# Optimization experiments

Hardware: AMD Instinct MI355X
Metric: run time of the kernel (lower is better)

The kernel has to match this reference:

```python
import jax, jax.numpy as jnp
import numpy as np

B, H, S, D = 4, 16, 2048, 128

def setup_inputs() -> dict:
    key = jax.random.key(0)
    kq, kk, kv = jax.random.split(key, 3)
    q = jax.random.normal(kq, (B, H, S, D), dtype=jnp.float32)
    k = jax.random.normal(kk, (B, H, S, D), dtype=jnp.float32)
    v = jax.random.normal(kv, (B, H, S, D), dtype=jnp.float32)
    # causal mask: True = masked (upper triangle above the diagonal)
    mask = jnp.triu(jnp.ones((S, S), dtype=jnp.bool_), k=1)[None, None, :, :]
    return {"q": q, "k": k, "v": v, "mask": mask}

def reference(q, k, v, mask):
    head_dim = q.shape[-1]
    scale = 1.0 / jnp.sqrt(jnp.float32(head_dim))
    # scores: [B, H, Sq, Sk]
    scores = jnp.einsum('bhqd,bhkd->bhqk', q, k) * scale
    scores = jnp.where(mask, -jnp.inf, scores)
    attention_weights = jax.nn.softmax(scores, axis=-1)
    # dropout p=0.0 (eval): identity
    context_vectors = jnp.einsum('bhqk,bhkd->bhqd', attention_weights, v)
    return (context_vectors, attention_weights)
```

## Files before the change

kernel.cpp:

```cpp
#include <hip/hip_runtime.h>
#include <hip/hip_bf16.h>

#define S_LEN 2048
#define D_DIM 128
#define BH_N  64
#define BR    64
#define BC    64
#define NTILE (S_LEN / BC)
#define SCALE 0.08838834764831845f
#define WB    256

typedef __attribute__((ext_vector_type(8)))  short short8;
typedef __attribute__((ext_vector_type(16))) float f32x16;

__device__ __forceinline__ ushort f2bf(float f) {
  union { float f; unsigned u; } x; x.f = f;
  unsigned r = x.u + 0x7FFFu + ((x.u >> 16) & 1u);
  return (ushort)(r >> 16);
}

__device__ __forceinline__ short8 pack8(float4 a, float4 b) {
  short8 p;
  p[0] = (short)f2bf(a.x); p[1] = (short)f2bf(a.y);
  p[2] = (short)f2bf(a.z); p[3] = (short)f2bf(a.w);
  p[4] = (short)f2bf(b.x); p[5] = (short)f2bf(b.y);
  p[6] = (short)f2bf(b.z); p[7] = (short)f2bf(b.w);
  return p;
}

__global__ __launch_bounds__(256, 2) void attn_flash_kernel(
    const float* __restrict__ q, const float* __restrict__ k,
    const float* __restrict__ v, float* __restrict__ ctx,
    float* __restrict__ lsum_out) {
  __shared__ __align__(16) char klds[BC * 256];
  __shared__ __align__(16) char vtlds[D_DIM * 128];
  __shared__ __align__(16) char plds[BR * 128];
  __shared__ float lred[2][BR];

  const int tid  = threadIdx.x;
  const int lane = tid & 63;
  const int w    = tid >> 6;
  const int wq   = w >> 1, wk = w & 1;
  const int l31  = lane & 31, lhi = lane >> 5;

  const int bid = blockIdx.x;
  const int qb  = (NTILE - 1) - (bid >> 6);
  const int bh  = bid & 63;

  const float* qbase = q + (size_t)bh * S_LEN * D_DIM;
  const float* kbase = k + (size_t)bh * S_LEN * D_DIM;
  const float* vbase = v + (size_t)bh * S_LEN * D_DIM;

  short8 qf[8];
  {
    const float* qrow = qbase + (size_t)(qb * BR + wq * 32 + l31) * D_DIM;
    #pragma unroll
    for (int s = 0; s < 8; ++s) {
      int d0 = 16 * s + 8 * lhi;
      float4 a = *(const float4*)(qrow + d0);
      float4 b = *(const float4*)(qrow + d0 + 4);
      qf[s] = pack8(a, b);
    }
  }

  float4 kreg[8], vreg[8];

  auto load_k = [&](int kt) {
    int trow = tid >> 2, tc = tid & 3;
    const float* src = kbase + (size_t)(kt * BC + trow) * D_DIM;
    #pragma unroll
    for (int i = 0; i < 4; ++i) {
      int c0 = tc * 8 + i * 32;
      kreg[2 * i]     = *(const float4*)(src + c0);
      kreg[2 * i + 1] = *(const float4*)(src + c0 + 4);
    }
  };
  auto write_k = [&]() {
    int trow = tid >> 2, tc = tid & 3;
    #pragma unroll
    for (int i = 0; i < 4; ++i) {
      int c0 = tc * 8 + i * 32;
      int off = (trow * 256 + c0 * 2) ^ ((trow & 7) << 4);
      *(short8*)(klds + off) = pack8(kreg[2 * i], kreg[2 * i + 1]);
    }
  };
  auto load_v = [&](int kt) {
    int kp = tid & 31, dg = tid >> 5;
    const float* r0 = vbase + (size_t)(kt * BC + 2 * kp) * D_DIM + dg * 16;
    #pragma unroll
    for (int i = 0; i < 4; ++i) {
      vreg[i]     = *(const float4*)(r0 + 4 * i);
      vreg[4 + i] = *(const float4*)(r0 + D_DIM + 4 * i);
    }
  };
  auto write_v = [&]() {
    int kp = tid & 31, dg = tid >> 5;
    #pragma unroll
    for (int j = 0; j < 16; ++j) {
      int d = dg * 16 + j;
      float lo = vreg[j >> 2][j & 3];
      float hi = vreg[4 + (j >> 2)][j & 3];
      unsigned u = (unsigned)f2bf(lo) | ((unsigned)f2bf(hi) << 16);
      int off = (d * 128 + kp * 4) ^ ((d & 7) << 4);
      *(unsigned*)(vtlds + off) = u;
    }
  };

  auto compute_s = [&]() -> f32x16 {
    f32x16 acc;
    #pragma unroll
    for (int i = 0; i < 16; ++i) acc[i] = 0.f;
    int krow = wk * 32 + l31;
    int base = krow * 256;
    int swz  = (krow & 7) << 4;
    #pragma unroll
    for (int s = 0; s < 8; ++s) {
      int off = (base + 32 * s + 16 * lhi) ^ swz;
      short8 kf = *(const short8*)(klds + off);
      acc = __builtin_amdgcn_mfma_f32_32x32x16_bf16(qf[s], kf, acc, 0, 0, 0);
    }
    return acc;
  };

  float l_lane[16];
  f32x16 o0, o1;
  #pragma unroll
  for (int i = 0; i < 16; ++i) { l_lane[i] = 0.f; o0[i] = 0.f; o1[i] = 0.f; }

  load_k(0); load_v(0);

  for (int kt = 0; kt <= qb; ++kt) {
    write_k(); write_v();
    if (kt < qb) { load_k(kt + 1); load_v(kt + 1); }
    __syncthreads();

    f32x16 acc = compute_s();
    int kcol_l = wk * 32 + l31;
    int kcol = kt * BC + kcol_l;
    bool diag = (kt == qb);
    #pragma unroll
    for (int r = 0; r < 16; ++r) {
      int rl = wq * 32 + (r & 3) + 8 * (r >> 2) + 4 * lhi;
      int qrow = qb * BR + rl;
      float e = (diag && kcol > qrow) ? 0.f : __expf(acc[r] * SCALE);
      l_lane[r] += e;
      int poff = (rl * 128 + kcol_l * 2) ^ ((rl & 7) << 4);
      *(ushort*)(plds + poff) = f2bf(e);
    }
    __syncthreads();

    #pragma unroll
    for (int s = 0; s < 4; ++s) {
      int prow = wq * 32 + l31;
      int paoff = (prow * 128 + (16 * s + 8 * lhi) * 2) ^ ((prow & 7) << 4);
      short8 pa = *(const short8*)(plds + paoff);
      int kko = (16 * s + 8 * lhi) * 2;
      int d0 = wk * 64 + l31;
      int d1 = d0 + 32;
      int off0 = (d0 * 128 + kko) ^ ((d0 & 7) << 4);
      int off1 = (d1 * 128 + kko) ^ ((d1 & 7) << 4);
      short8 vb0 = *(const short8*)(vtlds + off0);
      short8 vb1 = *(const short8*)(vtlds + off1);
      o0 = __builtin_amdgcn_mfma_f32_32x32x16_bf16(pa, vb0, o0, 0, 0, 0);
      o1 = __builtin_amdgcn_mfma_f32_32x32x16_bf16(pa, vb1, o1, 0, 0, 0);
    }
    __syncthreads();
  }

  #pragma unroll
  for (int r = 0; r < 16; ++r) {
    float x = l_lane[r];
    x += __shfl_xor(x, 1);  x += __shfl_xor(x, 2);  x += __shfl_xor(x, 4);
    x += __shfl_xor(x, 8);  x += __shfl_xor(x, 16);
    l_lane[r] = x;
  }
  if (l31 == 0) {
    #pragma unroll
    for (int r = 0; r < 16; ++r) {
      int rl = wq * 32 + (r & 3) + 8 * (r >> 2) + 4 * lhi;
      lred[wk][rl] = l_lane[r];
    }
  }
  __syncthreads();

  if (tid < BR)
    lsum_out[(size_t)bh * S_LEN + qb * BR + tid] = lred[0][tid] + lred[1][tid];

  float inv_l[16];
  #pragma unroll
  for (int r = 0; r < 16; ++r) {
    int rl = wq * 32 + (r & 3) + 8 * (r >> 2) + 4 * lhi;
    inv_l[r] = 1.0f / (lred[0][rl] + lred[1][rl]);
  }
  #pragma unroll
  for (int r = 0; r < 16; ++r) {
    int rl = wq * 32 + (r & 3) + 8 * (r >> 2) + 4 * lhi;
    size_t obase = (size_t)(bh * S_LEN + qb * BR + rl) * D_DIM;
    ctx[obase + wk * 64 + l31]      = o0[r] * inv_l[r];
    ctx[obase + wk * 64 + 32 + l31] = o1[r] * inv_l[r];
  }
}

__global__ __launch_bounds__(256, 2) void attn_wts2_kernel(
    const float* __restrict__ q, const float* __restrict__ k,
    const float* __restrict__ lsum, float* __restrict__ wts) {
  __shared__ __align__(16) float pslab[64 * WB];

  const int tid  = threadIdx.x;
  const int lane = tid & 63;
  const int w    = tid >> 6;
  const int wq   = w >> 1, wk = w & 1;
  const int l31  = lane & 31, lhi = lane >> 5;

  const int bid   = blockIdx.x;
  const int bh    = bid & 63;
  const int panel = (NTILE - 1) - (bid >> 6);

  float* wtile = wts + ((size_t)(bh * S_LEN + panel * BR)) * S_LEN;
  const int nslab = panel / 4 + 1;
  const int rowmax = panel * BR + BR - 1;

  short8 qf[8];
  {
    const float* qrow = q + (size_t)(bh * S_LEN + panel * BR + wq * 32 + l31) * D_DIM;
    #pragma unroll
    for (int s = 0; s < 8; ++s) {
      int d0 = 16 * s + 8 * lhi;
      float4 a = *(const float4*)(qrow + d0);
      float4 b = *(const float4*)(qrow + d0 + 4);
      qf[s] = pack8(a, b);
    }
  }

  float invl[16];
  #pragma unroll
  for (int r = 0; r < 16; ++r) {
    int rl = wq * 32 + (r & 3) + 8 * (r >> 2) + 4 * lhi;
    invl[r] = 1.0f / lsum[(size_t)bh * S_LEN + panel * BR + rl];
  }

  const float* kbase = k + (size_t)bh * S_LEN * D_DIM;

  for (int s = 0; s < nslab; ++s) {
    #pragma unroll
    for (int cb = 0; cb < 4; ++cb) {
      const int colb = s * WB + wk * 128 + cb * 32;
      const int col_local = wk * 128 + cb * 32 + l31;
      if (colb > rowmax) {
        #pragma unroll
        for (int r = 0; r < 16; ++r) {
          int rl = wq * 32 + (r & 3) + 8 * (r >> 2) + 4 * lhi;
          pslab[rl * WB + col_local] = 0.f;
        }
        continue;
      }
      const float* krow = kbase + (size_t)(colb + l31) * D_DIM;
      f32x16 acc;
      #pragma unroll
      for (int i = 0; i < 16; ++i) acc[i] = 0.f;
      #pragma unroll
      for (int s8 = 0; s8 < 8; ++s8) {
        int d0 = 16 * s8 + 8 * lhi;
        float4 a = *(const float4*)(krow + d0);
        float4 b = *(const float4*)(krow + d0 + 4);
        short8 kf = pack8(a, b);
        acc = __builtin_amdgcn_mfma_f32_32x32x16_bf16(qf[s8], kf, acc, 0, 0, 0);
      }
      const int cg = colb + l31;
      #pragma unroll
      for (int r = 0; r < 16; ++r) {
        int rl = wq * 32 + (r & 3) + 8 * (r >> 2) + 4 * lhi;
        int rowg = panel * BR + rl;
        float p = (cg > rowg) ? 0.f : __expf(acc[r] * SCALE) * invl[r];
        pslab[rl * WB + col_local] = p;
      }
    }
    __syncthreads();
    #pragma unroll
    for (int pass = 0; pass < 16; ++pass) {
      int row = pass * 4 + w;
      float4 val = *(const float4*)&pslab[row * WB + lane * 4];
      *(float4*)(wtile + (size_t)row * S_LEN + s * WB + lane * 4) = val;
    }
    __syncthreads();
  }

  float4 z; z.x = z.y = z.z = z.w = 0.f;
  for (int s = nslab; s < S_LEN / WB; ++s) {
    #pragma unroll
    for (int pass = 0; pass < 16; ++pass) {
      int row = pass * 4 + w;
      *(float4*)(wtile + (size_t)row * S_LEN + s * WB + lane * 4) = z;
    }
  }
}

extern "C" void kernel_launch(void* const* d_in, const int* in_sizes, int n_in,
                              void* d_out, int out_size, void* d_ws, size_t ws_size,
                              hipStream_t stream) {
  const float* q = (const float*)d_in[0];
  const float* k = (const float*)d_in[1];
  const float* v = (const float*)d_in[2];
  float* ctx = (float*)d_out;
  float* wts = ctx + (size_t)BH_N * S_LEN * D_DIM;
  float* lsum = (float*)d_ws;

  attn_flash_kernel<<<dim3(BH_N * NTILE), dim3(256), 0, stream>>>(q, k, v, ctx, lsum);
  attn_wts2_kernel<<<dim3(BH_N * NTILE), dim3(256), 0, stream>>>(q, k, lsum, wts);
}
```

Measured before the change: 569.9 us.

## Pre-convert K to bf16, split weights kernel into per-slab blocks, separate zero fill

Adds a pre-pass that converts K to bf16 in workspace, so the flash and weights kernels load half the bytes and skip per-element packing. The weights kernel is re-gridded so each block handles one 256-column slab of one panel, which raises parallelism and removes per-slab syncs. Upper-triangle zero filling moves to its own kernel, and the large weight writes use nontemporal stores. This costs an extra pass over K and one more launch, and it depends on having enough workspace, with a fallback path otherwise.

```diff
diff --git a/kernel.cpp b/kernel.cpp
--- a/kernel.cpp
+++ b/kernel.cpp
@@ -9,9 +9,13 @@
 #define NTILE (S_LEN / BC)
 #define SCALE 0.08838834764831845f
 #define WB    256
+#define SD    (S_LEN * D_DIM)
+#define LSUM_BYTES (BH_N * S_LEN * 4)
+#define WS_NEED (LSUM_BYTES + (size_t)BH_N * SD * 2)
 
 typedef __attribute__((ext_vector_type(8)))  short short8;
 typedef __attribute__((ext_vector_type(16))) float f32x16;
+typedef __attribute__((ext_vector_type(4)))  float fv4;
 
 __device__ __forceinline__ ushort f2bf(float f) {
   union { float f; unsigned u; } x; x.f = f;
@@ -28,10 +32,22 @@
   return p;
 }
 
+__global__ __launch_bounds__(256) void cvt_k_kernel(
+    const float* __restrict__ k, ushort* __restrict__ kb) {
+  size_t total = (size_t)BH_N * SD / 8;
+  for (size_t i = (size_t)blockIdx.x * 256 + threadIdx.x; i < total;
+       i += (size_t)gridDim.x * 256) {
+    float4 a = *(const float4*)(k + i * 8);
+    float4 b = *(const float4*)(k + i * 8 + 4);
+    *(short8*)(kb + i * 8) = pack8(a, b);
+  }
+}
+
+template <bool KB16>
 __global__ __launch_bounds__(256, 2) void attn_flash_kernel(
     const float* __restrict__ q, const float* __restrict__ k,
-    const float* __restrict__ v, float* __restrict__ ctx,
-    float* __restrict__ lsum_out) {
+    const ushort* __restrict__ kb, const float* __restrict__ v,
+    float* __restrict__ ctx, float* __restrict__ lsum_out) {
   __shared__ __align__(16) char klds[BC * 256];
   __shared__ __align__(16) char vtlds[D_DIM * 128];
   __shared__ __align__(16) char plds[BR * 128];
@@ -47,9 +63,10 @@
   const int qb  = (NTILE - 1) - (bid >> 6);
   const int bh  = bid & 63;
 
-  const float* qbase = q + (size_t)bh * S_LEN * D_DIM;
-  const float* kbase = k + (size_t)bh * S_LEN * D_DIM;
-  const float* vbase = v + (size_t)bh * S_LEN * D_DIM;
+  const float*  qbase  = q  + (size_t)bh * SD;
+  const float*  kbase  = k  + (size_t)bh * SD;
+  const ushort* kbbase = kb + (size_t)bh * SD;
+  const float*  vbase  = v  + (size_t)bh * SD;
 
   short8 qf[8];
   {
@@ -64,15 +81,23 @@
   }
 
   float4 kreg[8], vreg[8];
+  short8 kreg16[4];
 
   auto load_k = [&](int kt) {
     int trow = tid >> 2, tc = tid & 3;
-    const float* src = kbase + (size_t)(kt * BC + trow) * D_DIM;
-    #pragma unroll
-    for (int i = 0; i < 4; ++i) {
-      int c0 = tc * 8 + i * 32;
-      kreg[2 * i]     = *(const float4*)(src + c0);
-      kreg[2 * i + 1] = *(const float4*)(src + c0 + 4);
+    if constexpr (KB16) {
+      const ushort* src = kbbase + (size_t)(kt * BC + trow) * D_DIM;
+      #pragma unroll
+      for (int i = 0; i < 4; ++i)
+        kreg16[i] = *(const short8*)(src + tc * 8 + i * 32);
+    } else {
+      const float* src = kbase + (size_t)(kt * BC + trow) * D_DIM;
+      #pragma unroll
+      for (int i = 0; i < 4; ++i) {
+        int c0 = tc * 8 + i * 32;
+        kreg[2 * i]     = *(const float4*)(src + c0);
+        kreg[2 * i + 1] = *(const float4*)(src + c0 + 4);
+      }
     }
   };
   auto write_k = [&]() {
@@ -81,7 +106,10 @@
     for (int i = 0; i < 4; ++i) {
       int c0 = tc * 8 + i * 32;
       int off = (trow * 256 + c0 * 2) ^ ((trow & 7) << 4);
-      *(short8*)(klds + off) = pack8(kreg[2 * i], kreg[2 * i + 1]);
+      if constexpr (KB16)
+        *(short8*)(klds + off) = kreg16[i];
+      else
+        *(short8*)(klds + off) = pack8(kreg[2 * i], kreg[2 * i + 1]);
     }
   };
   auto load_v = [&](int kt) {
@@ -201,10 +229,18 @@
   }
 }
 
-__global__ __launch_bounds__(256, 2) void attn_wts2_kernel(
+template <bool KB16>
+__global__ __launch_bounds__(256, 2) void attn_wts_slab_kernel(
     const float* __restrict__ q, const float* __restrict__ k,
-    const float* __restrict__ lsum, float* __restrict__ wts) {
+    const ushort* __restrict__ kb, const float* __restrict__ lsum,
+    float* __restrict__ wts) {
   __shared__ __align__(16) float pslab[64 * WB];
+
+  const int bid   = blockIdx.x;
+  const int s     = bid & 7;
+  const int panel = (bid >> 3) & 31;
+  const int bh    = bid >> 8;
+  if (s > (panel >> 2)) return;
 
   const int tid  = threadIdx.x;
   const int lane = tid & 63;
@@ -212,23 +248,18 @@
   const int wq   = w >> 1, wk = w & 1;
   const int l31  = lane & 31, lhi = lane >> 5;
 
-  const int bid   = blockIdx.x;
-  const int bh    = bid & 63;
-  const int panel = (NTILE - 1) - (bid >> 6);
-
-  float* wtile = wts + ((size_t)(bh * S_LEN + panel * BR)) * S_LEN;
-  const int nslab = panel / 4 + 1;
   const int rowmax = panel * BR + BR - 1;
+  float* wtile = wts + ((size_t)(bh * S_LEN + panel * BR)) * S_LEN + s * WB;
 
   short8 qf[8];
   {
     const float* qrow = q + (size_t)(bh * S_LEN + panel * BR + wq * 32 + l31) * D_DIM;
     #pragma unroll
-    for (int s = 0; s < 8; ++s) {
-      int d0 = 16 * s + 8 * lhi;
+    for (int i = 0; i < 8; ++i) {
+      int d0 = 16 * i + 8 * lhi;
       float4 a = *(const float4*)(qrow + d0);
       float4 b = *(const float4*)(qrow + d0 + 4);
-      qf[s] = pack8(a, b);
+      qf[i] = pack8(a, b);
     }
   }
 
@@ -239,25 +270,30 @@
     invl[r] = 1.0f / lsum[(size_t)bh * S_LEN + panel * BR + rl];
   }
 
-  const float* kbase = k + (size_t)bh * S_LEN * D_DIM;
-
-  for (int s = 0; s < nslab; ++s) {
-    #pragma unroll
-    for (int cb = 0; cb < 4; ++cb) {
-      const int colb = s * WB + wk * 128 + cb * 32;
-      const int col_local = wk * 128 + cb * 32 + l31;
-      if (colb > rowmax) {
-        #pragma unroll
-        for (int r = 0; r < 16; ++r) {
-          int rl = wq * 32 + (r & 3) + 8 * (r >> 2) + 4 * lhi;
-          pslab[rl * WB + col_local] = 0.f;
-        }
-        continue;
+  #pragma unroll
+  for (int cb = 0; cb < 4; ++cb) {
+    const int colb = s * WB + wk * 128 + cb * 32;
+    const int col_local = wk * 128 + cb * 32 + l31;
+    if (colb > rowmax) {
+      #pragma unroll
+      for (int r = 0; r < 16; ++r) {
+        int rl = wq * 32 + (r & 3) + 8 * (r >> 2) + 4 * lhi;
+        pslab[rl * WB + col_local] = 0.f;
       }
-      const float* krow = kbase + (size_t)(colb + l31) * D_DIM;
-      f32x16 acc;
-      #pragma unroll
-      for (int i = 0; i < 16; ++i) acc[i] = 0.f;
+      continue;
+    }
+    f32x16 acc;
+    #pragma unroll
+    for (int i = 0; i < 16; ++i) acc[i] = 0.f;
+    if constexpr (KB16) {
+      const ushort* krow = kb + (size_t)bh * SD + (size_t)(colb + l31) * D_DIM;
+      #pragma unroll
+      for (int s8 = 0; s8 < 8; ++s8) {
+        short8 kf = *(const short8*)(krow + 16 * s8 + 8 * lhi);
+        acc = __builtin_amdgcn_mfma_f32_32x32x16_bf16(qf[s8], kf, acc, 0, 0, 0);
+      }
+    } else {
+      const float* krow = k + (size_t)bh * SD + (size_t)(colb + l31) * D_DIM;
       #pragma unroll
       for (int s8 = 0; s8 < 8; ++s8) {
         int d0 = 16 * s8 + 8 * lhi;
@@ -266,31 +302,42 @@
         short8 kf = pack8(a, b);
         acc = __builtin_amdgcn_mfma_f32_32x32x16_bf16(qf[s8], kf, acc, 0, 0, 0);
       }
-      const int cg = colb + l31;
-      #pragma unroll
-      for (int r = 0; r < 16; ++r) {
-        int rl = wq * 32 + (r & 3) + 8 * (r >> 2) + 4 * lhi;
-        int rowg = panel * BR + rl;
-        float p = (cg > rowg) ? 0.f : __expf(acc[r] * SCALE) * invl[r];
-        pslab[rl * WB + col_local] = p;
-      }
-    }
-    __syncthreads();
+    }
+    const int cg = colb + l31;
+    #pragma unroll
+    for (int r = 0; r < 16; ++r) {
+      int rl = wq * 32 + (r & 3) + 8 * (r >> 2) + 4 * lhi;
+      int rowg = panel * BR + rl;
+      float p = (cg > rowg) ? 0.f : __expf(acc[r] * SCALE) * invl[r];
+      pslab[rl * WB + col_local] = p;
+    }
+  }
+  __syncthreads();
+  #pragma unroll
+  for (int pass = 0; pass < 16; ++pass) {
+    int row = pass * 4 + w;
+    fv4 val = *(const fv4*)&pslab[row * WB + lane * 4];
+    __builtin_nontemporal_store(val, (fv4*)(wtile + (size_t)row * S_LEN + lane * 4));
+  }
+}
+
+__global__ __launch_bounds__(256) void attn_wts_zero_kernel(float* __restrict__ wts) {
+  const int bid   = blockIdx.x;
+  const int bh    = bid & 63;
+  const int panel = bid >> 6;
+  const int s0    = (panel >> 2) + 1;
+  const int tid   = threadIdx.x;
+  const int lane  = tid & 63;
+  const int w     = tid >> 6;
+
+  float* wtile = wts + ((size_t)(bh * S_LEN + panel * BR)) * S_LEN;
+  fv4 z = (fv4)0.f;
+  for (int s = s0; s < S_LEN / WB; ++s) {
     #pragma unroll
     for (int pass = 0; pass < 16; ++pass) {
       int row = pass * 4 + w;
-      float4 val = *(const float4*)&pslab[row * WB + lane * 4];
-      *(float4*)(wtile + (size_t)row * S_LEN + s * WB + lane * 4) = val;
-    }
-    __syncthreads();
-  }
-
-  float4 z; z.x = z.y = z.z = z.w = 0.f;
-  for (int s = nslab; s < S_LEN / WB; ++s) {
-    #pragma unroll
-    for (int pass = 0; pass < 16; ++pass) {
-      int row = pass * 4 + w;
-      *(float4*)(wtile + (size_t)row * S_LEN + s * WB + lane * 4) = z;
+      __builtin_nontemporal_store(
+          z, (fv4*)(wtile + (size_t)row * S_LEN + s * WB + lane * 4));
     }
   }
 }
@@ -302,9 +349,23 @@
   const float* k = (const float*)d_in[1];
   const float* v = (const float*)d_in[2];
   float* ctx = (float*)d_out;
-  float* wts = ctx + (size_t)BH_N * S_LEN * D_DIM;
-  float* lsum = (float*)d_ws;
-
-  attn_flash_kernel<<<dim3(BH_N * NTILE), dim3(256), 0, stream>>>(q, k, v, ctx, lsum);
-  attn_wts2_kernel<<<dim3(BH_N * NTILE), dim3(256), 0, stream>>>(q, k, lsum, wts);
-}
+  float* wts = ctx + (size_t)BH_N * SD;
+  float*  lsum = (float*)d_ws;
+  ushort* kb16 = (ushort*)((char*)d_ws + LSUM_BYTES);
+
+  const bool fast = ws_size >= WS_NEED;
+
+  if (fast) {
+    cvt_k_kernel<<<dim3(2048), dim3(256), 0, stream>>>(k, kb16);
+    attn_flash_kernel<true><<<dim3(BH_N * NTILE), dim3(256), 0, stream>>>(
+        q, k, kb16, v, ctx, lsum);
+    attn_wts_slab_kernel<true><<<dim3(BH_N * NTILE * 8), dim3(256), 0, stream>>>(
+        q, k, kb16, lsum, wts);
+  } else {
+    attn_flash_kernel<false><<<dim3(BH_N * NTILE), dim3(256), 0, stream>>>(
+        q, k, kb16, v, ctx, lsum);
+    attn_wts_slab_kernel<false><<<dim3(BH_N * NTILE * 8), dim3(256), 0, stream>>>(
+        q, k, kb16, lsum, wts);
+  }
+  attn_wts_zero_kernel<<<dim3(BH_N * NTILE), dim3(256), 0, stream>>>(wts);
+}
```

Measured after the change: 683.0 us. +19.8%, slower.
